# Kernel tuning notes

Hardware: AMD Instinct MI355X
Metric: run time of the kernel (lower is better)

Reference implementation:

```python
import jax, jax.numpy as jnp
import numpy as np
from jax import lax
import math

B, C, H, W, HEADS = 4, 64, 48, 48, 4
CH = C * HEADS
EPS_IN = 1e-5   # InstanceNorm2d eps
EPS_LN = 1e-5   # LayerNorm eps
EPS_NRM = 1e-12 # F.normalize eps


def setup_inputs() -> dict:
    key = jax.random.key(0)
    ks = jax.random.split(key, 8)
    rn = lambda k, shape, s: (jax.random.normal(k, shape, jnp.float32) * s)
    return {
        "emb_all": jax.random.normal(ks[0], (B, C, H, W), jnp.float32),
        "ln_w": jnp.ones((C,), jnp.float32),
        "ln_b": jnp.zeros((C,), jnp.float32),
        "wq": rn(ks[1], (CH, C), 0.05),
        "wk": rn(ks[2], (CH, C), 0.05),
        "wv": rn(ks[3], (CH, C), 0.05),
        "dwq": rn(ks[4], (CH, 1, 3, 3), 0.1),
        "dwk": rn(ks[5], (CH, 1, 3, 3), 0.1),
        "dwv": rn(ks[6], (CH, 1, 3, 3), 0.1),
        "proj_w": rn(ks[7], (C, C), 0.05),
        "proj_b": jnp.zeros((C,), jnp.float32),
    }


def _layernorm_c(x, w, b):
    # Restormer-style 'WithBias' LayerNorm over channel dim of NCHW
    mu = jnp.mean(x, axis=1, keepdims=True)
    var = jnp.mean((x - mu) ** 2, axis=1, keepdims=True)
    xn = (x - mu) / jnp.sqrt(var + EPS_LN)
    return xn * w[None, :, None, None] + b[None, :, None, None]


def _dwconv3(x, k):
    # depthwise 3x3, padding=1, NCHW / OIHW
    return lax.conv_general_dilated(
        x, k, window_strides=(1, 1), padding="SAME",
        feature_group_count=CH,
        dimension_numbers=("NCHW", "OIHW", "NCHW"))


def _qkv_branch(x, w1x1, dw):
    y = jnp.einsum("bchw,oc->bohw", x, w1x1)          # 1x1 conv, no bias
    y = _dwconv3(y, dw)                                # depthwise 3x3
    # b (head c) h w -> b head (h w) c
    y = y.reshape(B, HEADS, C, H * W).transpose(0, 1, 3, 2)
    return y


def reference(emb_all, ln_w, ln_b, wq, wk, wv, dwq, dwk, dwv, proj_w, proj_b):
    org = emb_all
    x = _layernorm_c(emb_all, ln_w, ln_b)

    q = _qkv_branch(x, wq, dwq)   # (B, HEADS, HW, C)
    k = _qkv_branch(x, wk, dwk)
    v = _qkv_branch(x, wv, dwv)

    # L2-normalize along channel dim (F.normalize semantics)
    q = q / jnp.maximum(jnp.linalg.norm(q, axis=-1, keepdims=True), EPS_NRM)
    k = k / jnp.maximum(jnp.linalg.norm(k, axis=-1, keepdims=True), EPS_NRM)

    num = H * W
    atten = jnp.einsum("bhnc,bhmc->bhnm", q, k) / math.sqrt(num)

    # InstanceNorm2d over the (hw x hw) score map, per (batch, head), no affine
    mu = jnp.mean(atten, axis=(-2, -1), keepdims=True)
    var = jnp.mean((atten - mu) ** 2, axis=(-2, -1), keepdims=True)
    atten = (atten - mu) / jnp.sqrt(var + EPS_IN)

    probs = jax.nn.softmax(atten, axis=-1)

    out = jnp.einsum("bhnm,bhmc->bhnc", probs, v)      # (B, HEADS, HW, C)
    out = out.mean(axis=1)                             # average over heads
    out = out.transpose(0, 2, 1).reshape(B, C, H, W)   # b (h w) c -> b c h w
    out = jnp.einsum("bchw,oc->bohw", out, proj_w) + proj_b[None, :, None, None]
    return org + out
```

## Files before the change

kernel.cpp:

```cpp
#include <hip/hip_runtime.h>
#include <hip/hip_bf16.h>
#include <math.h>

#define NB 4
#define NC 64
#define NH 48
#define NW 48
#define NHEADS 4
#define NCH 256
#define NHW 2304
#define NBH 16
#define NCHK 4
#define CHUNK 576
#define NT (CHUNK / 32)

#define OB_Y    0ull
#define OB_G    0ull
#define OB_SQ   524288ull
#define OB_OHP  0ull
#define OB_Q    18874368ull
#define OB_K    23592960ull
#define OB_V    28311552ull
#define OB_L    33030144ull
#define OB_SC   33619968ull

typedef __bf16 bf16x8 __attribute__((ext_vector_type(8)));
typedef float f32x4 __attribute__((ext_vector_type(4)));
typedef float f32x16 __attribute__((ext_vector_type(16)));

__device__ __forceinline__ float bf2f(ushort u) {
  return __uint_as_float(((unsigned)u) << 16);
}
__device__ __forceinline__ ushort f2bf(float f) {
  __hip_bfloat16 h = __float2bfloat16(f);
  return *(ushort*)&h;
}
__device__ __forceinline__ void gload16(const void* g, void* l) {
  __builtin_amdgcn_global_load_lds((const __attribute__((address_space(1))) unsigned int*)g,
                                   (__attribute__((address_space(3))) unsigned int*)l, 16, 0, 0);
}

__global__ __launch_bounds__(256) void k_lnconv(const float* __restrict__ emb,
                                                const float* __restrict__ lw,
                                                const float* __restrict__ lb,
                                                const float* __restrict__ wq,
                                                const float* __restrict__ wk,
                                                const float* __restrict__ wv,
                                                ushort* __restrict__ Y) {
  __shared__ float Xs[64][68];
  __shared__ float mu_s[64], rs_s[64], lw_s[64], lb_s[64];
  int p0 = blockIdx.x * 64, b = blockIdx.y, qkv = blockIdx.z;
  const float* Wm = qkv == 0 ? wq : (qkv == 1 ? wk : wv);
  const float* src = emb + (size_t)b * NC * NHW + p0;
  int t = threadIdx.x;
  for (int e = t; e < 1024; e += 256) {
    int c = e >> 4, p4 = (e & 15) * 4;
    float4 v = *(const float4*)&src[c * NHW + p4];
    Xs[p4][c] = v.x; Xs[p4 + 1][c] = v.y; Xs[p4 + 2][c] = v.z; Xs[p4 + 3][c] = v.w;
  }
  if (t < 64) { lw_s[t] = lw[t]; lb_s[t] = lb[t]; }
  __syncthreads();
  if (t < 64) {
    float s = 0.f, ss = 0.f;
#pragma unroll
    for (int c = 0; c < 64; c += 4) {
      float4 v = *(const float4*)&Xs[t][c];
      s += (v.x + v.y) + (v.z + v.w);
      ss += (v.x * v.x + v.y * v.y) + (v.z * v.z + v.w * v.w);
    }
    float m = s * (1.f / 64.f), va = ss * (1.f / 64.f) - m * m;
    mu_s[t] = m;
    rs_s[t] = rsqrtf(va + 1e-5f);
  }
  __syncthreads();
  int lane = t & 63, wvi = t >> 6, ql = lane & 31, h = lane >> 5;
  bf16x8 bfr[2][4];
#pragma unroll
  for (int pb = 0; pb < 2; ++pb) {
    int px = pb * 32 + ql;
    float mu = mu_s[px], rs = rs_s[px];
#pragma unroll
    for (int kc = 0; kc < 4; ++kc) {
      union { bf16x8 v; ushort u[8]; } pk;
#pragma unroll
      for (int j = 0; j < 8; ++j) {
        int c = kc * 16 + h * 8 + j;
        pk.u[j] = f2bf((Xs[px][c] - mu) * rs * lw_s[c] + lb_s[c]);
      }
      bfr[pb][kc] = pk.v;
    }
  }
  bf16x8 afr[2][4];
#pragma unroll
  for (int ob = 0; ob < 2; ++ob) {
    const float* wr = Wm + (size_t)(wvi * 64 + ob * 32 + ql) * 64;
#pragma unroll
    for (int kc = 0; kc < 4; ++kc) {
      union { bf16x8 v; ushort u[8]; } pk;
#pragma unroll
      for (int j = 0; j < 8; ++j) pk.u[j] = f2bf(wr[kc * 16 + h * 8 + j]);
      afr[ob][kc] = pk.v;
    }
  }
  f32x16 d00 = {}, d01 = {}, d10 = {}, d11 = {};
#pragma unroll
  for (int kc = 0; kc < 4; ++kc) {
    d00 = __builtin_amdgcn_mfma_f32_32x32x16_bf16(afr[0][kc], bfr[0][kc], d00, 0, 0, 0);
    d01 = __builtin_amdgcn_mfma_f32_32x32x16_bf16(afr[0][kc], bfr[1][kc], d01, 0, 0, 0);
    d10 = __builtin_amdgcn_mfma_f32_32x32x16_bf16(afr[1][kc], bfr[0][kc], d10, 0, 0, 0);
    d11 = __builtin_amdgcn_mfma_f32_32x32x16_bf16(afr[1][kc], bfr[1][kc], d11, 0, 0, 0);
  }
  ushort* dst = Y + ((size_t)(qkv * NB + b) * NCH + wvi * 64) * NHW + p0;
#pragma unroll
  for (int r = 0; r < 16; ++r) {
    int row = (r & 3) + 8 * (r >> 2) + 4 * h;
    dst[(size_t)row * NHW + ql] = f2bf(d00[r]);
    dst[(size_t)row * NHW + 32 + ql] = f2bf(d01[r]);
    dst[(size_t)(32 + row) * NHW + ql] = f2bf(d10[r]);
    dst[(size_t)(32 + row) * NHW + 32 + ql] = f2bf(d11[r]);
  }
}

__global__ __launch_bounds__(256) void k_dw(const ushort* __restrict__ Y,
                                            const float* __restrict__ dwq,
                                            const float* __restrict__ dwk,
                                            const float* __restrict__ dwv,
                                            ushort* __restrict__ Qo,
                                            ushort* __restrict__ Ko,
                                            ushort* __restrict__ Vo) {
  __shared__ ushort Ys[64][3][48];
  __shared__ float Zs[64][50];
  __shared__ float Ks9[64][9];
  __shared__ float Rp[4][48];
  __shared__ float Rs[48];
  int h = blockIdx.x;
  int hd = blockIdx.y & 3, qkv = blockIdx.y >> 2;
  int b = blockIdx.z;
  int bh = b * NHEADS + hd;
  const float* dwp = qkv == 0 ? dwq : (qkv == 1 ? dwk : dwv);
  const ushort* src = Y + ((size_t)(qkv * NB + b) * NCH + hd * 64) * NHW;
  int t = threadIdx.x;
  for (int e = t; e < 576; e += 256) Ks9[e / 9][e % 9] = dwp[(size_t)hd * 576 + e];
  for (int e = t; e < 2304; e += 256) {
    int c = e / 36, rem = e % 36, r = rem / 12, w4 = (rem % 12) * 4;
    int hh = h + r - 1;
    ushort4 v = (hh >= 0 && hh < NH) ? *(const ushort4*)&src[c * NHW + hh * NW + w4]
                                     : make_ushort4(0, 0, 0, 0);
    *(ushort4*)&Ys[c][r][w4] = v;
  }
  __syncthreads();
  for (int e = t; e < 768; e += 256) {
    int c = e / 12, w4 = (e % 12) * 4;
    float acc0 = 0.f, acc1 = 0.f, acc2 = 0.f, acc3 = 0.f;
#pragma unroll
    for (int r = 0; r < 3; ++r) {
      const ushort* row = &Ys[c][r][0];
      int li = w4 >= 4 ? w4 - 4 : 0;
      int ri = w4 <= 40 ? w4 + 4 : 40;
      uint2 L = *(const uint2*)&row[li];
      uint2 M = *(const uint2*)&row[w4];
      uint2 R = *(const uint2*)&row[ri];
      float vm1 = (w4 == 0) ? 0.f : __uint_as_float(L.y & 0xffff0000u);
      float m0 = __uint_as_float(M.x << 16);
      float m1 = __uint_as_float(M.x & 0xffff0000u);
      float m2 = __uint_as_float(M.y << 16);
      float m3 = __uint_as_float(M.y & 0xffff0000u);
      float v4 = (w4 == 44) ? 0.f : __uint_as_float(R.x << 16);
      float k0 = Ks9[c][r * 3], k1 = Ks9[c][r * 3 + 1], k2 = Ks9[c][r * 3 + 2];
      acc0 += vm1 * k0 + m0 * k1 + m1 * k2;
      acc1 += m0 * k0 + m1 * k1 + m2 * k2;
      acc2 += m1 * k0 + m2 * k1 + m3 * k2;
      acc3 += m2 * k0 + m3 * k1 + v4 * k2;
    }
    *(float2*)&Zs[c][w4] = make_float2(acc0, acc1);
    *(float2*)&Zs[c][w4 + 2] = make_float2(acc2, acc3);
  }
  __syncthreads();
  if (qkv < 2) {
    if (t < 192) {
      int cq = t / 48, w = t % 48;
      float ss = 0.f;
#pragma unroll
      for (int i = 0; i < 16; ++i) { float z = Zs[cq * 16 + i][w]; ss += z * z; }
      Rp[cq][w] = ss;
    }
    __syncthreads();
    if (t < 48)
      Rs[t] = 1.f / fmaxf(sqrtf(Rp[0][t] + Rp[1][t] + Rp[2][t] + Rp[3][t]), 1e-12f);
    __syncthreads();
    ushort* dst = (qkv == 0 ? Qo : Ko) + (size_t)bh * NHW * 64;
    for (int e = t; e < 768; e += 256) {
      int w = e >> 4, c4 = (e & 15) * 4;
      float rsc = Rs[w];
      ushort4 u = make_ushort4(f2bf(Zs[c4][w] * rsc), f2bf(Zs[c4 + 1][w] * rsc),
                               f2bf(Zs[c4 + 2][w] * rsc), f2bf(Zs[c4 + 3][w] * rsc));
      *(ushort4*)&dst[((size_t)(c4 >> 3) * NHW + h * NW + w) * 8 + (c4 & 7)] = u;
    }
  } else {
    ushort* dst = Vo + (size_t)bh * NHW * 64;
    for (int e = t; e < 768; e += 256) {
      int c = e / 12, w4 = (e % 12) * 4;
      float4 z = *(const float4*)&Zs[c][w4];
      ushort4 u = make_ushort4(f2bf(z.x), f2bf(z.y), f2bf(z.z), f2bf(z.w));
      *(ushort4*)&dst[((size_t)(h * 6 + (w4 >> 3)) * 64 + c) * 8 + (w4 & 7)] = u;
    }
  }
}

__global__ __launch_bounds__(256) void k_gram(const ushort* __restrict__ Q,
                                              const ushort* __restrict__ K,
                                              float* __restrict__ G,
                                              float* __restrict__ SQ) {
  __shared__ ushort Xt[64][72];
  int ns = blockIdx.x, qk = blockIdx.y, bh = blockIdx.z;
  const ushort* src = (qk ? K : Q) + (size_t)bh * NHW * 64;
  int t = threadIdx.x, lane = t & 63, wv = t >> 6;
  int lr = lane & 15, lg = lane >> 4;
  int ci0 = (wv >> 1) * 32, cj0 = (wv & 1) * 32;
  f32x4 acc[2][2];
#pragma unroll
  for (int i = 0; i < 2; ++i)
#pragma unroll
    for (int j = 0; j < 2; ++j) acc[i][j] = (f32x4){0.f, 0.f, 0.f, 0.f};
  float sq = 0.f;
  for (int it = 0; it < 4; ++it) {
    __syncthreads();
#pragma unroll
    for (int i2 = 0; i2 < 2; ++i2) {
      int n = t & 63, cg = (t >> 6) + 4 * i2;
      union { bf16x8 v; ushort u[8]; } ld;
      ld.v = *(const bf16x8*)&src[((size_t)cg * NHW + ns * 256 + it * 64 + n) * 8];
#pragma unroll
      for (int j = 0; j < 8; ++j) Xt[cg * 8 + j][n] = ld.u[j];
    }
    __syncthreads();
    if (t < 64) {
#pragma unroll
      for (int g = 0; g < 8; ++g) {
        union { bf16x8 v; ushort u[8]; } rd;
        rd.v = *(const bf16x8*)&Xt[t][g * 8];
#pragma unroll
        for (int j = 0; j < 8; ++j) sq += bf2f(rd.u[j]);
      }
    }
#pragma unroll
    for (int kh = 0; kh < 2; ++kh) {
      bf16x8 a0 = *(const bf16x8*)&Xt[ci0 + lr][kh * 32 + lg * 8];
      bf16x8 a1 = *(const bf16x8*)&Xt[ci0 + 16 + lr][kh * 32 + lg * 8];
      bf16x8 b0 = *(const bf16x8*)&Xt[cj0 + lr][kh * 32 + lg * 8];
      bf16x8 b1 = *(const bf16x8*)&Xt[cj0 + 16 + lr][kh * 32 + lg * 8];
      acc[0][0] = __builtin_amdgcn_mfma_f32_16x16x32_bf16(a0, b0, acc[0][0], 0, 0, 0);
      acc[0][1] = __builtin_amdgcn_mfma_f32_16x16x32_bf16(a0, b1, acc[0][1], 0, 0, 0);
      acc[1][0] = __builtin_amdgcn_mfma_f32_16x16x32_bf16(a1, b0, acc[1][0], 0, 0, 0);
      acc[1][1] = __builtin_amdgcn_mfma_f32_16x16x32_bf16(a1, b1, acc[1][1], 0, 0, 0);
    }
  }
  float* g = G + ((size_t)qk * NBH + bh) * 4096;
#pragma unroll
  for (int ii = 0; ii < 2; ++ii)
#pragma unroll
    for (int jj = 0; jj < 2; ++jj)
#pragma unroll
      for (int r = 0; r < 4; ++r)
        atomicAdd(&g[(ci0 + ii * 16 + lg * 4 + r) * 64 + cj0 + jj * 16 + lr], acc[ii][jj][r]);
  if (t < 64) atomicAdd(&SQ[((size_t)qk * NBH + bh) * 64 + t], sq);
}

__global__ __launch_bounds__(256) void k_scale(const float* __restrict__ G,
                                               const float* __restrict__ SQ,
                                               float* __restrict__ SC) {
  __shared__ float red[256];
  int bh = blockIdx.x, t = threadIdx.x;
  float ssum = 0.f;
  for (int i = t; i < 4096; i += 256)
    ssum += G[(size_t)bh * 4096 + i] * G[(size_t)(NBH + bh) * 4096 + i];
  red[t] = ssum;
  __syncthreads();
  if (t < 128) red[t] += red[t + 128];
  __syncthreads();
  if (t < 64) {
    float v = red[t] + red[t + 64];
    float v2 = SQ[bh * 64 + t] * SQ[(NBH + bh) * 64 + t];
#pragma unroll
    for (int m = 32; m; m >>= 1) { v += __shfl_xor(v, m); v2 += __shfl_xor(v2, m); }
    if (t == 0) {
      const double N2 = (double)NHW * (double)NHW;
      double mean = (double)v2 / (N2 * 48.0);
      double ea2 = (double)v / (N2 * 2304.0);
      double var = ea2 - mean * mean;
      SC[bh] = (float)((1.0 / sqrt(var + 1e-5)) / 48.0 * 1.4426950408889634);
    }
  }
}

__global__ __launch_bounds__(256, 2) void k_attn(const ushort* __restrict__ Q,
                                                 const ushort* __restrict__ K,
                                                 const ushort* __restrict__ V,
                                                 const float* __restrict__ SC,
                                                 ushort* __restrict__ OHp,
                                                 float* __restrict__ Lp) {
  __shared__ ushort Kl[4][2048];
  __shared__ ushort Vl[4][2048];
  int p = blockIdx.x;
  int gb = p & 7;
  int w = p >> 3;
  int qt = w % 18;
  int rem = w / 18;
  int chunk = rem & 3;
  int bh = gb * 2 + (rem >> 2);
  int t = threadIdx.x, lane = t & 63, wv = t >> 6;
  int ql = lane & 31, h = lane >> 5;
  int q0 = qt * 128 + wv * 32;
  int m00 = chunk * CHUNK;
  const ushort* base = Q + (size_t)bh * NHW * 64;
  float sc2 = SC[bh];

  bf16x8 qfr[4];
#pragma unroll
  for (int kc = 0; kc < 4; ++kc)
    qfr[kc] = *(const bf16x8*)&base[((size_t)(kc * 2 + h) * NHW + q0 + ql) * 8];
  asm volatile("s_waitcnt vmcnt(0)" ::: "memory");

  const ushort* kst = K + (size_t)bh * NHW * 64 + ((size_t)(wv * 2 + h) * NHW + m00 + ql) * 8;
  const ushort* vst = V + (size_t)bh * NHW * 64 + ((size_t)((m00 >> 3) + wv) * 64 + lane) * 8;

  f32x16 o0 = {}, o1 = {};
  float lpA = 0.f, lpB = 0.f;

  auto STAGE = [&](int tt) {
    gload16(kst + (size_t)tt * 256, (void*)&Kl[tt & 3][wv * 512]);
    gload16(vst + (size_t)tt * 2048, (void*)&Vl[tt & 3][wv * 512]);
  };
  auto COMPUTE = [&](int cb, float& lpr) {
    bf16x8 ka[4], vb[4];
#pragma unroll
    for (int i = 0; i < 4; ++i)
      ka[i] = *(const bf16x8*)&Kl[cb][(2 * i + h) * 256 + ql * 8];
    vb[0] = *(const bf16x8*)&Vl[cb][h * 512 + ql * 8];
    vb[1] = *(const bf16x8*)&Vl[cb][(2 + h) * 512 + ql * 8];
    vb[2] = *(const bf16x8*)&Vl[cb][h * 512 + (ql + 32) * 8];
    vb[3] = *(const bf16x8*)&Vl[cb][(2 + h) * 512 + (ql + 32) * 8];
    __builtin_amdgcn_s_setprio(1);
    f32x16 s = {};
    s = __builtin_amdgcn_mfma_f32_32x32x16_bf16(ka[0], qfr[0], s, 0, 0, 0);
    s = __builtin_amdgcn_mfma_f32_32x32x16_bf16(ka[1], qfr[1], s, 0, 0, 0);
    s = __builtin_amdgcn_mfma_f32_32x32x16_bf16(ka[2], qfr[2], s, 0, 0, 0);
    s = __builtin_amdgcn_mfma_f32_32x32x16_bf16(ka[3], qfr[3], s, 0, 0, 0);
    __builtin_amdgcn_s_setprio(0);
    float pv[16];
    float l0 = 0.f, l1 = 0.f, l2 = 0.f, l3 = 0.f;
#pragma unroll
    for (int r = 0; r < 16; r += 4) {
      pv[r] = __builtin_exp2f(s[r] * sc2);
      pv[r + 1] = __builtin_exp2f(s[r + 1] * sc2);
      pv[r + 2] = __builtin_exp2f(s[r + 2] * sc2);
      pv[r + 3] = __builtin_exp2f(s[r + 3] * sc2);
      l0 += pv[r]; l1 += pv[r + 1]; l2 += pv[r + 2]; l3 += pv[r + 3];
    }
    lpr += (l0 + l1) + (l2 + l3);
    uint u[8];
#pragma unroll
    for (int i = 0; i < 8; ++i)
      asm("v_cvt_pk_bf16_f32 %0, %1, %2" : "=v"(u[i]) : "v"(pv[2 * i]), "v"(pv[2 * i + 1]));
    asm volatile("v_permlane32_swap_b32 %0, %1" : "+v"(u[0]), "+v"(u[2]));
    asm volatile("v_permlane32_swap_b32 %0, %1" : "+v"(u[1]), "+v"(u[3]));
    asm volatile("v_permlane32_swap_b32 %0, %1" : "+v"(u[4]), "+v"(u[6]));
    asm volatile("v_permlane32_swap_b32 %0, %1" : "+v"(u[5]), "+v"(u[7]));
    union { uint uu[4]; bf16x8 v; } pa0, pa1;
    pa0.uu[0] = u[0]; pa0.uu[1] = u[1]; pa0.uu[2] = u[2]; pa0.uu[3] = u[3];
    pa1.uu[0] = u[4]; pa1.uu[1] = u[5]; pa1.uu[2] = u[6]; pa1.uu[3] = u[7];
    __builtin_amdgcn_s_setprio(1);
    o0 = __builtin_amdgcn_mfma_f32_32x32x16_bf16(pa0.v, vb[0], o0, 0, 0, 0);
    o0 = __builtin_amdgcn_mfma_f32_32x32x16_bf16(pa1.v, vb[1], o0, 0, 0, 0);
    o1 = __builtin_amdgcn_mfma_f32_32x32x16_bf16(pa0.v, vb[2], o1, 0, 0, 0);
    o1 = __builtin_amdgcn_mfma_f32_32x32x16_bf16(pa1.v, vb[3], o1, 0, 0, 0);
    __builtin_amdgcn_s_setprio(0);
  };

  STAGE(0); STAGE(1);
  for (int mt = 0; mt < NT; mt += 2) {
    asm volatile("s_waitcnt vmcnt(0)" ::: "memory");
    __builtin_amdgcn_s_barrier();
    if (mt + 2 < NT) { STAGE(mt + 2); STAGE(mt + 3); }
    COMPUTE(mt & 3, lpA);
    COMPUTE((mt + 1) & 3, lpB);
  }

  float lp = lpA + lpB;
  lp += __shfl_xor(lp, 32);
  if (h == 0) Lp[(size_t)(chunk * NBH + bh) * NHW + q0 + ql] = lp;
  ushort* od = OHp + ((size_t)(chunk * NBH + bh) * NHW + q0) * 64;
#pragma unroll
  for (int r = 0; r < 16; ++r) {
    int qrow = (r & 3) + 8 * (r >> 2) + 4 * h;
    od[(size_t)qrow * 64 + ql] = f2bf(o0[r]);
    od[(size_t)qrow * 64 + 32 + ql] = f2bf(o1[r]);
  }
}

__global__ __launch_bounds__(256) void k_proj(const ushort* __restrict__ OHp,
                                              const float* __restrict__ Lp,
                                              const float* __restrict__ PW,
                                              const float* __restrict__ PB,
                                              const float* __restrict__ org,
                                              float* __restrict__ out) {
  __shared__ float Ls[4][4][16];
  __shared__ float linv[4][16];
  __shared__ float Ms[64][17];
  int p0 = blockIdx.x * 16, b = blockIdx.y;
  int t = threadIdx.x;
  {
    int ck = t >> 6, hd = (t >> 4) & 3, p = t & 15;
    Ls[ck][hd][p] = Lp[(size_t)(ck * NBH + b * 4 + hd) * NHW + p0 + p];
  }
  __syncthreads();
  if (t < 64) {
    int hd = t >> 4, p = t & 15;
    linv[hd][p] = 1.f / (Ls[0][hd][p] + Ls[1][hd][p] + Ls[2][hd][p] + Ls[3][hd][p]);
  }
  __syncthreads();
  {
    int p = t >> 4, c4 = (t & 15) * 4;
    float a0 = 0.f, a1 = 0.f, a2 = 0.f, a3 = 0.f;
#pragma unroll
    for (int hd = 0; hd < 4; ++hd) {
      float s0 = 0.f, s1 = 0.f, s2 = 0.f, s3 = 0.f;
#pragma unroll
      for (int ck = 0; ck < 4; ++ck) {
        ushort4 u = *(const ushort4*)&OHp[((size_t)(ck * NBH + b * 4 + hd) * NHW + p0 + p) * 64 + c4];
        s0 += bf2f(u.x); s1 += bf2f(u.y); s2 += bf2f(u.z); s3 += bf2f(u.w);
      }
      float li = linv[hd][p];
      a0 += s0 * li; a1 += s1 * li; a2 += s2 * li; a3 += s3 * li;
    }
    Ms[c4][p] = 0.25f * a0;
    Ms[c4 + 1][p] = 0.25f * a1;
    Ms[c4 + 2][p] = 0.25f * a2;
    Ms[c4 + 3][p] = 0.25f * a3;
  }
  __syncthreads();
  int p = t & 15, og = t >> 4;
  float acc[4];
#pragma unroll
  for (int i = 0; i < 4; ++i) acc[i] = PB[og * 4 + i];
  for (int c = 0; c < 64; ++c) {
    float xr = Ms[c][p];
#pragma unroll
    for (int i = 0; i < 4; ++i) acc[i] += PW[(og * 4 + i) * 64 + c] * xr;
  }
  const float* orgp = org + (size_t)b * NC * NHW + p0 + p;
  float* outp = out + (size_t)b * NC * NHW + p0 + p;
#pragma unroll
  for (int i = 0; i < 4; ++i) {
    int oc = og * 4 + i;
    outp[(size_t)oc * NHW] = orgp[(size_t)oc * NHW] + acc[i];
  }
}

extern "C" void kernel_launch(void* const* d_in, const int* in_sizes, int n_in,
                              void* d_out, int out_size, void* d_ws, size_t ws_size,
                              hipStream_t stream) {
  const float* emb = (const float*)d_in[0];
  const float* lnw = (const float*)d_in[1];
  const float* lnb = (const float*)d_in[2];
  const float* wq  = (const float*)d_in[3];
  const float* wk  = (const float*)d_in[4];
  const float* wv  = (const float*)d_in[5];
  const float* dwq = (const float*)d_in[6];
  const float* dwk = (const float*)d_in[7];
  const float* dwv = (const float*)d_in[8];
  const float* pw  = (const float*)d_in[9];
  const float* pb  = (const float*)d_in[10];
  char* ws = (char*)d_ws;
  ushort* Y   = (ushort*)(ws + OB_Y);
  float*  G   = (float*)(ws + OB_G);
  float*  SQ  = (float*)(ws + OB_SQ);
  ushort* OHp = (ushort*)(ws + OB_OHP);
  ushort* Qb  = (ushort*)(ws + OB_Q);
  ushort* Kb  = (ushort*)(ws + OB_K);
  ushort* Vb  = (ushort*)(ws + OB_V);
  float*  Lpt = (float*)(ws + OB_L);
  float*  SCp = (float*)(ws + OB_SC);
  float* out = (float*)d_out;

  k_lnconv<<<dim3(NHW / 64, NB, 3), 256, 0, stream>>>(emb, lnw, lnb, wq, wk, wv, Y);
  k_dw<<<dim3(NH, 12, NB), 256, 0, stream>>>(Y, dwq, dwk, dwv, Qb, Kb, Vb);
  hipMemsetAsync(G, 0, 532480, stream);
  k_gram<<<dim3(9, 2, NBH), 256, 0, stream>>>(Qb, Kb, G, SQ);
  k_scale<<<dim3(NBH), 256, 0, stream>>>(G, SQ, SCp);
  k_attn<<<dim3(1152), 256, 0, stream>>>(Qb, Kb, Vb, SCp, OHp, Lpt);
  k_proj<<<dim3(NHW / 16, NB), 256, 0, stream>>>(OHp, Lpt, pw, pb, emb, out);
}
```

Baseline: 108.7 us.

## Enlarge attention blocks to 8 waves sharing K/V tiles with split loaders

The attention kernel now uses 512-thread blocks covering 256 queries, so each staged K/V tile is reused by eight waves instead of four. Half the waves load K and half load V, one load each per tile. The pipeline moves from double-tile steps with a full vmcnt(0) wait to single-tile steps with a partial vmcnt wait, keeping two tiles in flight. This cuts global K/V traffic and LDS staging per query, at the cost of twice as many barriers and larger-block synchronisation.

```diff
diff --git a/kernel.cpp b/kernel.cpp
--- a/kernel.cpp
+++ b/kernel.cpp
@@ -293,7 +293,7 @@
   }
 }
 
-__global__ __launch_bounds__(256, 2) void k_attn(const ushort* __restrict__ Q,
+__global__ __launch_bounds__(512, 1) void k_attn(const ushort* __restrict__ Q,
                                                  const ushort* __restrict__ K,
                                                  const ushort* __restrict__ V,
                                                  const float* __restrict__ SC,
@@ -304,13 +304,13 @@
   int p = blockIdx.x;
   int gb = p & 7;
   int w = p >> 3;
-  int qt = w % 18;
-  int rem = w / 18;
+  int qt = w % 9;
+  int rem = w / 9;
   int chunk = rem & 3;
   int bh = gb * 2 + (rem >> 2);
   int t = threadIdx.x, lane = t & 63, wv = t >> 6;
   int ql = lane & 31, h = lane >> 5;
-  int q0 = qt * 128 + wv * 32;
+  int q0 = qt * 256 + wv * 32;
   int m00 = chunk * CHUNK;
   const ushort* base = Q + (size_t)bh * NHW * 64;
   float sc2 = SC[bh];
@@ -321,17 +321,21 @@
     qfr[kc] = *(const bf16x8*)&base[((size_t)(kc * 2 + h) * NHW + q0 + ql) * 8];
   asm volatile("s_waitcnt vmcnt(0)" ::: "memory");
 
-  const ushort* kst = K + (size_t)bh * NHW * 64 + ((size_t)(wv * 2 + h) * NHW + m00 + ql) * 8;
-  const ushort* vst = V + (size_t)bh * NHW * 64 + ((size_t)((m00 >> 3) + wv) * 64 + lane) * 8;
+  int sw = wv & 3;
+  bool isK = wv < 4;
+  const ushort* st = isK
+      ? K + (size_t)bh * NHW * 64 + ((size_t)(sw * 2 + h) * NHW + m00 + ql) * 8
+      : V + (size_t)bh * NHW * 64 + ((size_t)((m00 >> 3) + sw) * 64 + lane) * 8;
+  int tstride = isK ? 256 : 2048;
 
   f32x16 o0 = {}, o1 = {};
-  float lpA = 0.f, lpB = 0.f;
+  float lp = 0.f;
 
   auto STAGE = [&](int tt) {
-    gload16(kst + (size_t)tt * 256, (void*)&Kl[tt & 3][wv * 512]);
-    gload16(vst + (size_t)tt * 2048, (void*)&Vl[tt & 3][wv * 512]);
+    void* dst = isK ? (void*)&Kl[tt & 3][sw * 512] : (void*)&Vl[tt & 3][sw * 512];
+    gload16(st + (size_t)tt * tstride, dst);
   };
-  auto COMPUTE = [&](int cb, float& lpr) {
+  auto COMPUTE = [&](int cb) {
     bf16x8 ka[4], vb[4];
 #pragma unroll
     for (int i = 0; i < 4; ++i)
@@ -357,7 +361,7 @@
       pv[r + 3] = __builtin_exp2f(s[r + 3] * sc2);
       l0 += pv[r]; l1 += pv[r + 1]; l2 += pv[r + 2]; l3 += pv[r + 3];
     }
-    lpr += (l0 + l1) + (l2 + l3);
+    lp += (l0 + l1) + (l2 + l3);
     uint u[8];
 #pragma unroll
     for (int i = 0; i < 8; ++i)
@@ -378,15 +382,19 @@
   };
 
   STAGE(0); STAGE(1);
-  for (int mt = 0; mt < NT; mt += 2) {
-    asm volatile("s_waitcnt vmcnt(0)" ::: "memory");
+  for (int mt = 0; mt < NT; ++mt) {
+    if (mt + 2 < NT) {
+      STAGE(mt + 2);
+      asm volatile("s_waitcnt vmcnt(2)" ::: "memory");
+    } else if (mt + 1 < NT) {
+      asm volatile("s_waitcnt vmcnt(1)" ::: "memory");
+    } else {
+      asm volatile("s_waitcnt vmcnt(0)" ::: "memory");
+    }
     __builtin_amdgcn_s_barrier();
-    if (mt + 2 < NT) { STAGE(mt + 2); STAGE(mt + 3); }
-    COMPUTE(mt & 3, lpA);
-    COMPUTE((mt + 1) & 3, lpB);
-  }
-
-  float lp = lpA + lpB;
+    COMPUTE(mt & 3);
+  }
+
   lp += __shfl_xor(lp, 32);
   if (h == 0) Lp[(size_t)(chunk * NBH + bh) * NHW + q0 + ql] = lp;
   ushort* od = OHp + ((size_t)(chunk * NBH + bh) * NHW + q0) * 64;
@@ -488,6 +496,6 @@
   hipMemsetAsync(G, 0, 532480, stream);
   k_gram<<<dim3(9, 2, NBH), 256, 0, stream>>>(Qb, Kb, G, SQ);
   k_scale<<<dim3(NBH), 256, 0, stream>>>(G, SQ, SCp);
-  k_attn<<<dim3(1152), 256, 0, stream>>>(Qb, Kb, Vb, SCp, OHp, Lpt);
+  k_attn<<<dim3(576), 512, 0, stream>>>(Qb, Kb, Vb, SCp, OHp, Lpt);
   k_proj<<<dim3(NHW / 16, NB), 256, 0, stream>>>(OHp, Lpt, pw, pb, emb, out);
 }
```

Result: slower. 111.3 us (+2.4%).

## Fuse layernorm, 1x1 conv, depthwise conv and gram into one kernel; re-pipeline attention loads

Applied to the files above, without the earlier changes.

Merges the layernorm+1x1 conv, depthwise 3x3 conv and Q/K gram-matrix kernels into a single per-row kernel. Each block recomputes the 1x1 conv for its three input rows (a halo of 3 rows per output row), which removes the Y intermediate round trip through global memory and two launches. The gram partials are now accumulated per row with atomics. In exchange the block uses a large LDS pool, which may lower occupancy, and issues more atomic adds. The attention kernel also switches to a single-tile steady-state prefetch loop with a finer vmcnt wait.

```diff
diff --git a/kernel.cpp b/kernel.cpp
--- a/kernel.cpp
+++ b/kernel.cpp
@@ -14,7 +14,6 @@
 #define CHUNK 576
 #define NT (CHUNK / 32)
 
-#define OB_Y    0ull
 #define OB_G    0ull
 #define OB_SQ   524288ull
 #define OB_OHP  0ull
@@ -40,113 +39,126 @@
                                    (__attribute__((address_space(3))) unsigned int*)l, 16, 0, 0);
 }
 
-__global__ __launch_bounds__(256) void k_lnconv(const float* __restrict__ emb,
-                                                const float* __restrict__ lw,
-                                                const float* __restrict__ lb,
-                                                const float* __restrict__ wq,
-                                                const float* __restrict__ wk,
-                                                const float* __restrict__ wv,
-                                                ushort* __restrict__ Y) {
-  __shared__ float Xs[64][68];
-  __shared__ float mu_s[64], rs_s[64], lw_s[64], lb_s[64];
-  int p0 = blockIdx.x * 64, b = blockIdx.y, qkv = blockIdx.z;
-  const float* Wm = qkv == 0 ? wq : (qkv == 1 ? wk : wv);
-  const float* src = emb + (size_t)b * NC * NHW + p0;
-  int t = threadIdx.x;
-  for (int e = t; e < 1024; e += 256) {
-    int c = e >> 4, p4 = (e & 15) * 4;
-    float4 v = *(const float4*)&src[c * NHW + p4];
-    Xs[p4][c] = v.x; Xs[p4 + 1][c] = v.y; Xs[p4 + 2][c] = v.z; Xs[p4 + 3][c] = v.w;
-  }
-  if (t < 64) { lw_s[t] = lw[t]; lb_s[t] = lb[t]; }
-  __syncthreads();
-  if (t < 64) {
-    float s = 0.f, ss = 0.f;
-#pragma unroll
-    for (int c = 0; c < 64; c += 4) {
-      float4 v = *(const float4*)&Xs[t][c];
-      s += (v.x + v.y) + (v.z + v.w);
-      ss += (v.x * v.x + v.y * v.y) + (v.z * v.z + v.w * v.w);
-    }
-    float m = s * (1.f / 64.f), va = ss * (1.f / 64.f) - m * m;
-    mu_s[t] = m;
-    rs_s[t] = rsqrtf(va + 1e-5f);
-  }
-  __syncthreads();
-  int lane = t & 63, wvi = t >> 6, ql = lane & 31, h = lane >> 5;
-  bf16x8 bfr[2][4];
-#pragma unroll
-  for (int pb = 0; pb < 2; ++pb) {
-    int px = pb * 32 + ql;
-    float mu = mu_s[px], rs = rs_s[px];
-#pragma unroll
-    for (int kc = 0; kc < 4; ++kc) {
-      union { bf16x8 v; ushort u[8]; } pk;
-#pragma unroll
-      for (int j = 0; j < 8; ++j) {
-        int c = kc * 16 + h * 8 + j;
-        pk.u[j] = f2bf((Xs[px][c] - mu) * rs * lw_s[c] + lb_s[c]);
-      }
-      bfr[pb][kc] = pk.v;
-    }
-  }
-  bf16x8 afr[2][4];
-#pragma unroll
-  for (int ob = 0; ob < 2; ++ob) {
-    const float* wr = Wm + (size_t)(wvi * 64 + ob * 32 + ql) * 64;
-#pragma unroll
-    for (int kc = 0; kc < 4; ++kc) {
-      union { bf16x8 v; ushort u[8]; } pk;
-#pragma unroll
-      for (int j = 0; j < 8; ++j) pk.u[j] = f2bf(wr[kc * 16 + h * 8 + j]);
-      afr[ob][kc] = pk.v;
-    }
-  }
-  f32x16 d00 = {}, d01 = {}, d10 = {}, d11 = {};
-#pragma unroll
-  for (int kc = 0; kc < 4; ++kc) {
-    d00 = __builtin_amdgcn_mfma_f32_32x32x16_bf16(afr[0][kc], bfr[0][kc], d00, 0, 0, 0);
-    d01 = __builtin_amdgcn_mfma_f32_32x32x16_bf16(afr[0][kc], bfr[1][kc], d01, 0, 0, 0);
-    d10 = __builtin_amdgcn_mfma_f32_32x32x16_bf16(afr[1][kc], bfr[0][kc], d10, 0, 0, 0);
-    d11 = __builtin_amdgcn_mfma_f32_32x32x16_bf16(afr[1][kc], bfr[1][kc], d11, 0, 0, 0);
-  }
-  ushort* dst = Y + ((size_t)(qkv * NB + b) * NCH + wvi * 64) * NHW + p0;
-#pragma unroll
-  for (int r = 0; r < 16; ++r) {
-    int row = (r & 3) + 8 * (r >> 2) + 4 * h;
-    dst[(size_t)row * NHW + ql] = f2bf(d00[r]);
-    dst[(size_t)row * NHW + 32 + ql] = f2bf(d01[r]);
-    dst[(size_t)(32 + row) * NHW + ql] = f2bf(d10[r]);
-    dst[(size_t)(32 + row) * NHW + 32 + ql] = f2bf(d11[r]);
-  }
-}
-
-__global__ __launch_bounds__(256) void k_dw(const ushort* __restrict__ Y,
-                                            const float* __restrict__ dwq,
-                                            const float* __restrict__ dwk,
-                                            const float* __restrict__ dwv,
-                                            ushort* __restrict__ Qo,
-                                            ushort* __restrict__ Ko,
-                                            ushort* __restrict__ Vo) {
-  __shared__ ushort Ys[64][3][48];
-  __shared__ float Zs[64][50];
-  __shared__ float Ks9[64][9];
-  __shared__ float Rp[4][48];
-  __shared__ float Rs[48];
+#define PO_XB 39168
+#define PO_ZS 39168
+#define PO_RP 52768
+#define PO_RS 53536
+#define PO_K9 57600
+#define PO_MU 59904
+#define PO_RSD 60480
+#define PO_LW 61056
+#define PO_LB 61312
+__global__ __launch_bounds__(256) void k_qkv(const float* __restrict__ emb,
+                                             const float* __restrict__ lw,
+                                             const float* __restrict__ lb,
+                                             const float* __restrict__ wq,
+                                             const float* __restrict__ wk,
+                                             const float* __restrict__ wv,
+                                             const float* __restrict__ dwq,
+                                             const float* __restrict__ dwk,
+                                             const float* __restrict__ dwv,
+                                             ushort* __restrict__ Qo,
+                                             ushort* __restrict__ Ko,
+                                             ushort* __restrict__ Vo,
+                                             float* __restrict__ G,
+                                             float* __restrict__ SQ) {
+  __shared__ __align__(16) char pool[61952];
+  float* Xs = (float*)pool;
+  ushort* Yl = (ushort*)pool;
+  float* Zs = (float*)(pool + PO_ZS);
+  float* Rp = (float*)(pool + PO_RP);
+  float* Rs = (float*)(pool + PO_RS);
+  float* Ks9 = (float*)(pool + PO_K9);
+  float* mu_s = (float*)(pool + PO_MU);
+  float* rs_s = (float*)(pool + PO_RSD);
+  float* lw_s = (float*)(pool + PO_LW);
+  float* lb_s = (float*)(pool + PO_LB);
+
   int h = blockIdx.x;
   int hd = blockIdx.y & 3, qkv = blockIdx.y >> 2;
   int b = blockIdx.z;
   int bh = b * NHEADS + hd;
+  const float* Wm = qkv == 0 ? wq : (qkv == 1 ? wk : wv);
   const float* dwp = qkv == 0 ? dwq : (qkv == 1 ? dwk : dwv);
-  const ushort* src = Y + ((size_t)(qkv * NB + b) * NCH + hd * 64) * NHW;
-  int t = threadIdx.x;
-  for (int e = t; e < 576; e += 256) Ks9[e / 9][e % 9] = dwp[(size_t)hd * 576 + e];
+  int t = threadIdx.x, lane = t & 63, wvi = t >> 6;
+  int l15 = lane & 15, l4 = lane >> 4;
+
   for (int e = t; e < 2304; e += 256) {
     int c = e / 36, rem = e % 36, r = rem / 12, w4 = (rem % 12) * 4;
     int hh = h + r - 1;
-    ushort4 v = (hh >= 0 && hh < NH) ? *(const ushort4*)&src[c * NHW + hh * NW + w4]
-                                     : make_ushort4(0, 0, 0, 0);
-    *(ushort4*)&Ys[c][r][w4] = v;
+    float4 v = (hh >= 0 && hh < NH) ? *(const float4*)&emb[((size_t)b * NC + c) * NHW + hh * NW + w4]
+                                    : make_float4(0.f, 0.f, 0.f, 0.f);
+    int p = r * 48 + w4;
+    Xs[p * 68 + c] = v.x;
+    Xs[(p + 1) * 68 + c] = v.y;
+    Xs[(p + 2) * 68 + c] = v.z;
+    Xs[(p + 3) * 68 + c] = v.w;
+  }
+  if (t < 64) { lw_s[t] = lw[t]; lb_s[t] = lb[t]; }
+  for (int e = t; e < 576; e += 256) Ks9[e] = dwp[(size_t)hd * 576 + e];
+  __syncthreads();
+  if (t < 144) {
+    float s = 0.f, ss = 0.f;
+#pragma unroll
+    for (int c = 0; c < 64; c += 4) {
+      float4 v = *(const float4*)&Xs[t * 68 + c];
+      s += (v.x + v.y) + (v.z + v.w);
+      ss += (v.x * v.x + v.y * v.y) + (v.z * v.z + v.w * v.w);
+    }
+    float m = s * (1.f / 64.f), va = ss * (1.f / 64.f) - m * m;
+    mu_s[t] = m;
+    rs_s[t] = rsqrtf(va + 1e-5f);
+  }
+  __syncthreads();
+  for (int e = t; e < 1152; e += 256) {
+    int px = e >> 3, c8 = (e & 7) * 8;
+    int chunk = (c8 >> 3) ^ (px & 7);
+    float mu = mu_s[px], rs = rs_s[px];
+    float4 v0 = *(const float4*)&Xs[px * 68 + c8];
+    float4 v1 = *(const float4*)&Xs[px * 68 + c8 + 4];
+    union { bf16x8 v; ushort u[8]; } pk;
+    pk.u[0] = f2bf((v0.x - mu) * rs * lw_s[c8] + lb_s[c8]);
+    pk.u[1] = f2bf((v0.y - mu) * rs * lw_s[c8 + 1] + lb_s[c8 + 1]);
+    pk.u[2] = f2bf((v0.z - mu) * rs * lw_s[c8 + 2] + lb_s[c8 + 2]);
+    pk.u[3] = f2bf((v0.w - mu) * rs * lw_s[c8 + 3] + lb_s[c8 + 3]);
+    pk.u[4] = f2bf((v1.x - mu) * rs * lw_s[c8 + 4] + lb_s[c8 + 4]);
+    pk.u[5] = f2bf((v1.y - mu) * rs * lw_s[c8 + 5] + lb_s[c8 + 5]);
+    pk.u[6] = f2bf((v1.z - mu) * rs * lw_s[c8 + 6] + lb_s[c8 + 6]);
+    pk.u[7] = f2bf((v1.w - mu) * rs * lw_s[c8 + 7] + lb_s[c8 + 7]);
+    *(bf16x8*)(pool + PO_XB + px * 128 + chunk * 16) = pk.v;
+  }
+  __syncthreads();
+  {
+    bf16x8 afr[2];
+    const float* wr = Wm + (size_t)(hd * 64 + wvi * 16 + l15) * 64;
+#pragma unroll
+    for (int kc = 0; kc < 2; ++kc) {
+      float4 w0 = *(const float4*)&wr[kc * 32 + l4 * 8];
+      float4 w1 = *(const float4*)&wr[kc * 32 + l4 * 8 + 4];
+      union { bf16x8 v; ushort u[8]; } pk;
+      pk.u[0] = f2bf(w0.x); pk.u[1] = f2bf(w0.y); pk.u[2] = f2bf(w0.z); pk.u[3] = f2bf(w0.w);
+      pk.u[4] = f2bf(w1.x); pk.u[5] = f2bf(w1.y); pk.u[6] = f2bf(w1.z); pk.u[7] = f2bf(w1.w);
+      afr[kc] = pk.v;
+    }
+    f32x4 acc[9];
+#pragma unroll
+    for (int i = 0; i < 9; ++i) acc[i] = (f32x4){0.f, 0.f, 0.f, 0.f};
+#pragma unroll
+    for (int pxt = 0; pxt < 9; ++pxt) {
+      int px = pxt * 16 + l15;
+#pragma unroll
+      for (int kc = 0; kc < 2; ++kc) {
+        int chunk = (kc * 4 + l4) ^ (px & 7);
+        bf16x8 bfr = *(const bf16x8*)(pool + PO_XB + px * 128 + chunk * 16);
+        acc[pxt] = __builtin_amdgcn_mfma_f32_16x16x32_bf16(afr[kc], bfr, acc[pxt], 0, 0, 0);
+      }
+    }
+    __syncthreads();
+#pragma unroll
+    for (int pxt = 0; pxt < 9; ++pxt)
+#pragma unroll
+      for (int r = 0; r < 4; ++r)
+        Yl[(wvi * 16 + l4 * 4 + r) * 148 + pxt * 16 + l15] = f2bf(acc[pxt][r]);
   }
   __syncthreads();
   for (int e = t; e < 768; e += 256) {
@@ -154,7 +166,8 @@
     float acc0 = 0.f, acc1 = 0.f, acc2 = 0.f, acc3 = 0.f;
 #pragma unroll
     for (int r = 0; r < 3; ++r) {
-      const ushort* row = &Ys[c][r][0];
+      bool rOK = (unsigned)(h + r - 1) < (unsigned)NH;
+      const ushort* row = &Yl[c * 148 + r * 48];
       int li = w4 >= 4 ? w4 - 4 : 0;
       int ri = w4 <= 40 ? w4 + 4 : 40;
       uint2 L = *(const uint2*)&row[li];
@@ -166,14 +179,16 @@
       float m2 = __uint_as_float(M.y << 16);
       float m3 = __uint_as_float(M.y & 0xffff0000u);
       float v4 = (w4 == 44) ? 0.f : __uint_as_float(R.x << 16);
-      float k0 = Ks9[c][r * 3], k1 = Ks9[c][r * 3 + 1], k2 = Ks9[c][r * 3 + 2];
+      float k0 = rOK ? Ks9[c * 9 + r * 3] : 0.f;
+      float k1 = rOK ? Ks9[c * 9 + r * 3 + 1] : 0.f;
+      float k2 = rOK ? Ks9[c * 9 + r * 3 + 2] : 0.f;
       acc0 += vm1 * k0 + m0 * k1 + m1 * k2;
       acc1 += m0 * k0 + m1 * k1 + m2 * k2;
       acc2 += m1 * k0 + m2 * k1 + m3 * k2;
       acc3 += m2 * k0 + m3 * k1 + v4 * k2;
     }
-    *(float2*)&Zs[c][w4] = make_float2(acc0, acc1);
-    *(float2*)&Zs[c][w4 + 2] = make_float2(acc2, acc3);
+    *(float2*)&Zs[c * 50 + w4] = make_float2(acc0, acc1);
+    *(float2*)&Zs[c * 50 + w4 + 2] = make_float2(acc2, acc3);
   }
   __syncthreads();
   if (qkv < 2) {
@@ -181,89 +196,78 @@
       int cq = t / 48, w = t % 48;
       float ss = 0.f;
 #pragma unroll
-      for (int i = 0; i < 16; ++i) { float z = Zs[cq * 16 + i][w]; ss += z * z; }
-      Rp[cq][w] = ss;
+      for (int i = 0; i < 16; ++i) { float z = Zs[(cq * 16 + i) * 50 + w]; ss += z * z; }
+      Rp[cq * 48 + w] = ss;
     }
     __syncthreads();
     if (t < 48)
-      Rs[t] = 1.f / fmaxf(sqrtf(Rp[0][t] + Rp[1][t] + Rp[2][t] + Rp[3][t]), 1e-12f);
+      Rs[t] = 1.f / fmaxf(sqrtf(Rp[t] + Rp[48 + t] + Rp[96 + t] + Rp[144 + t]), 1e-12f);
     __syncthreads();
     ushort* dst = (qkv == 0 ? Qo : Ko) + (size_t)bh * NHW * 64;
     for (int e = t; e < 768; e += 256) {
       int w = e >> 4, c4 = (e & 15) * 4;
       float rsc = Rs[w];
-      ushort4 u = make_ushort4(f2bf(Zs[c4][w] * rsc), f2bf(Zs[c4 + 1][w] * rsc),
-                               f2bf(Zs[c4 + 2][w] * rsc), f2bf(Zs[c4 + 3][w] * rsc));
+      ushort4 u = make_ushort4(f2bf(Zs[c4 * 50 + w] * rsc), f2bf(Zs[(c4 + 1) * 50 + w] * rsc),
+                               f2bf(Zs[(c4 + 2) * 50 + w] * rsc), f2bf(Zs[(c4 + 3) * 50 + w] * rsc));
       *(ushort4*)&dst[((size_t)(c4 >> 3) * NHW + h * NW + w) * 8 + (c4 & 7)] = u;
+    }
+    for (int e = t; e < 384; e += 256) {
+      int c = e / 6, n8 = (e % 6) * 8;
+      int chunk = (n8 >> 3) ^ (c & 7);
+      union { bf16x8 v; ushort u[8]; } pk;
+#pragma unroll
+      for (int j = 0; j < 8; ++j) pk.u[j] = f2bf(Zs[c * 50 + n8 + j] * Rs[n8 + j]);
+      *(bf16x8*)(pool + c * 128 + chunk * 16) = pk.v;
+    }
+    for (int e = t; e < 128; e += 256) {
+      int c = e >> 1, ch = 6 + (e & 1);
+      int chunk = ch ^ (c & 7);
+      *(bf16x8*)(pool + c * 128 + chunk * 16) = (bf16x8){};
+    }
+    __syncthreads();
+    {
+      int ci0 = wvi * 16;
+      bf16x8 a[2];
+#pragma unroll
+      for (int kc = 0; kc < 2; ++kc) {
+        int row = ci0 + l15;
+        int chunk = (kc * 4 + l4) ^ (row & 7);
+        a[kc] = *(const bf16x8*)(pool + row * 128 + chunk * 16);
+      }
+      f32x4 g[4];
+#pragma unroll
+      for (int i = 0; i < 4; ++i) g[i] = (f32x4){0.f, 0.f, 0.f, 0.f};
+#pragma unroll
+      for (int cj = 0; cj < 4; ++cj) {
+        int row = cj * 16 + l15;
+#pragma unroll
+        for (int kc = 0; kc < 2; ++kc) {
+          int chunk = (kc * 4 + l4) ^ (row & 7);
+          bf16x8 bb = *(const bf16x8*)(pool + row * 128 + chunk * 16);
+          g[cj] = __builtin_amdgcn_mfma_f32_16x16x32_bf16(a[kc], bb, g[cj], 0, 0, 0);
+        }
+      }
+      float* gdst = G + ((size_t)qkv * NBH + bh) * 4096;
+#pragma unroll
+      for (int cj = 0; cj < 4; ++cj)
+#pragma unroll
+        for (int r = 0; r < 4; ++r)
+          atomicAdd(&gdst[(ci0 + l4 * 4 + r) * 64 + cj * 16 + l15], g[cj][r]);
+    }
+    if (t < 64) {
+      float s = 0.f;
+      for (int w = 0; w < 48; ++w) s += bf2f(f2bf(Zs[t * 50 + w] * Rs[w]));
+      atomicAdd(&SQ[((size_t)qkv * NBH + bh) * 64 + t], s);
     }
   } else {
     ushort* dst = Vo + (size_t)bh * NHW * 64;
     for (int e = t; e < 768; e += 256) {
       int c = e / 12, w4 = (e % 12) * 4;
-      float4 z = *(const float4*)&Zs[c][w4];
+      float4 z = *(const float4*)&Zs[c * 50 + w4];
       ushort4 u = make_ushort4(f2bf(z.x), f2bf(z.y), f2bf(z.z), f2bf(z.w));
       *(ushort4*)&dst[((size_t)(h * 6 + (w4 >> 3)) * 64 + c) * 8 + (w4 & 7)] = u;
     }
   }
-}
-
-__global__ __launch_bounds__(256) void k_gram(const ushort* __restrict__ Q,
-                                              const ushort* __restrict__ K,
-                                              float* __restrict__ G,
-                                              float* __restrict__ SQ) {
-  __shared__ ushort Xt[64][72];
-  int ns = blockIdx.x, qk = blockIdx.y, bh = blockIdx.z;
-  const ushort* src = (qk ? K : Q) + (size_t)bh * NHW * 64;
-  int t = threadIdx.x, lane = t & 63, wv = t >> 6;
-  int lr = lane & 15, lg = lane >> 4;
-  int ci0 = (wv >> 1) * 32, cj0 = (wv & 1) * 32;
-  f32x4 acc[2][2];
-#pragma unroll
-  for (int i = 0; i < 2; ++i)
-#pragma unroll
-    for (int j = 0; j < 2; ++j) acc[i][j] = (f32x4){0.f, 0.f, 0.f, 0.f};
-  float sq = 0.f;
-  for (int it = 0; it < 4; ++it) {
-    __syncthreads();
-#pragma unroll
-    for (int i2 = 0; i2 < 2; ++i2) {
-      int n = t & 63, cg = (t >> 6) + 4 * i2;
-      union { bf16x8 v; ushort u[8]; } ld;
-      ld.v = *(const bf16x8*)&src[((size_t)cg * NHW + ns * 256 + it * 64 + n) * 8];
-#pragma unroll
-      for (int j = 0; j < 8; ++j) Xt[cg * 8 + j][n] = ld.u[j];
-    }
-    __syncthreads();
-    if (t < 64) {
-#pragma unroll
-      for (int g = 0; g < 8; ++g) {
-        union { bf16x8 v; ushort u[8]; } rd;
-        rd.v = *(const bf16x8*)&Xt[t][g * 8];
-#pragma unroll
-        for (int j = 0; j < 8; ++j) sq += bf2f(rd.u[j]);
-      }
-    }
-#pragma unroll
-    for (int kh = 0; kh < 2; ++kh) {
-      bf16x8 a0 = *(const bf16x8*)&Xt[ci0 + lr][kh * 32 + lg * 8];
-      bf16x8 a1 = *(const bf16x8*)&Xt[ci0 + 16 + lr][kh * 32 + lg * 8];
-      bf16x8 b0 = *(const bf16x8*)&Xt[cj0 + lr][kh * 32 + lg * 8];
-      bf16x8 b1 = *(const bf16x8*)&Xt[cj0 + 16 + lr][kh * 32 + lg * 8];
-      acc[0][0] = __builtin_amdgcn_mfma_f32_16x16x32_bf16(a0, b0, acc[0][0], 0, 0, 0);
-      acc[0][1] = __builtin_amdgcn_mfma_f32_16x16x32_bf16(a0, b1, acc[0][1], 0, 0, 0);
-      acc[1][0] = __builtin_amdgcn_mfma_f32_16x16x32_bf16(a1, b0, acc[1][0], 0, 0, 0);
-      acc[1][1] = __builtin_amdgcn_mfma_f32_16x16x32_bf16(a1, b1, acc[1][1], 0, 0, 0);
-    }
-  }
-  float* g = G + ((size_t)qk * NBH + bh) * 4096;
-#pragma unroll
-  for (int ii = 0; ii < 2; ++ii)
-#pragma unroll
-    for (int jj = 0; jj < 2; ++jj)
-#pragma unroll
-      for (int r = 0; r < 4; ++r)
-        atomicAdd(&g[(ci0 + ii * 16 + lg * 4 + r) * 64 + cj0 + jj * 16 + lr], acc[ii][jj][r]);
-  if (t < 64) atomicAdd(&SQ[((size_t)qk * NBH + bh) * 64 + t], sq);
 }
 
 __global__ __launch_bounds__(256) void k_scale(const float* __restrict__ G,
@@ -325,13 +329,9 @@
   const ushort* vst = V + (size_t)bh * NHW * 64 + ((size_t)((m00 >> 3) + wv) * 64 + lane) * 8;
 
   f32x16 o0 = {}, o1 = {};
-  float lpA = 0.f, lpB = 0.f;
-
-  auto STAGE = [&](int tt) {
-    gload16(kst + (size_t)tt * 256, (void*)&Kl[tt & 3][wv * 512]);
-    gload16(vst + (size_t)tt * 2048, (void*)&Vl[tt & 3][wv * 512]);
-  };
-  auto COMPUTE = [&](int cb, float& lpr) {
+  float lp = 0.f;
+
+  auto COMPUTE = [&](int cb) {
     bf16x8 ka[4], vb[4];
 #pragma unroll
     for (int i = 0; i < 4; ++i)
@@ -357,7 +357,7 @@
       pv[r + 3] = __builtin_exp2f(s[r + 3] * sc2);
       l0 += pv[r]; l1 += pv[r + 1]; l2 += pv[r + 2]; l3 += pv[r + 3];
     }
-    lpr += (l0 + l1) + (l2 + l3);
+    lp += (l0 + l1) + (l2 + l3);
     uint u[8];
 #pragma unroll
     for (int i = 0; i < 8; ++i)
@@ -377,16 +377,26 @@
     __builtin_amdgcn_s_setprio(0);
   };
 
-  STAGE(0); STAGE(1);
-  for (int mt = 0; mt < NT; mt += 2) {
-    asm volatile("s_waitcnt vmcnt(0)" ::: "memory");
+  gload16(kst, (void*)&Kl[0][wv * 512]);
+  gload16(vst, (void*)&Vl[0][wv * 512]);
+  gload16(kst + 256, (void*)&Kl[1][wv * 512]);
+  gload16(vst + 2048, (void*)&Vl[1][wv * 512]);
+
+  for (int mt = 0; mt < NT - 2; ++mt) {
+    int sb = (mt + 2) & 3;
+    gload16(kst + (size_t)(mt + 2) * 256, (void*)&Kl[sb][wv * 512]);
+    gload16(vst + (size_t)(mt + 2) * 2048, (void*)&Vl[sb][wv * 512]);
+    asm volatile("s_waitcnt vmcnt(4)" ::: "memory");
     __builtin_amdgcn_s_barrier();
-    if (mt + 2 < NT) { STAGE(mt + 2); STAGE(mt + 3); }
-    COMPUTE(mt & 3, lpA);
-    COMPUTE((mt + 1) & 3, lpB);
-  }
-
-  float lp = lpA + lpB;
+    COMPUTE(mt & 3);
+  }
+  asm volatile("s_waitcnt vmcnt(2)" ::: "memory");
+  __builtin_amdgcn_s_barrier();
+  COMPUTE((NT - 2) & 3);
+  asm volatile("s_waitcnt vmcnt(0)" ::: "memory");
+  __builtin_amdgcn_s_barrier();
+  COMPUTE((NT - 1) & 3);
+
   lp += __shfl_xor(lp, 32);
   if (h == 0) Lp[(size_t)(chunk * NBH + bh) * NHW + q0 + ql] = lp;
   ushort* od = OHp + ((size_t)(chunk * NBH + bh) * NHW + q0) * 64;
@@ -472,7 +482,6 @@
   const float* pw  = (const float*)d_in[9];
   const float* pb  = (const float*)d_in[10];
   char* ws = (char*)d_ws;
-  ushort* Y   = (ushort*)(ws + OB_Y);
   float*  G   = (float*)(ws + OB_G);
   float*  SQ  = (float*)(ws + OB_SQ);
   ushort* OHp = (ushort*)(ws + OB_OHP);
@@ -483,10 +492,9 @@
   float*  SCp = (float*)(ws + OB_SC);
   float* out = (float*)d_out;
 
-  k_lnconv<<<dim3(NHW / 64, NB, 3), 256, 0, stream>>>(emb, lnw, lnb, wq, wk, wv, Y);
-  k_dw<<<dim3(NH, 12, NB), 256, 0, stream>>>(Y, dwq, dwk, dwv, Qb, Kb, Vb);
   hipMemsetAsync(G, 0, 532480, stream);
-  k_gram<<<dim3(9, 2, NBH), 256, 0, stream>>>(Qb, Kb, G, SQ);
+  k_qkv<<<dim3(NH, 12, NB), 256, 0, stream>>>(emb, lnw, lnb, wq, wk, wv, dwq, dwk, dwv,
+                                              Qb, Kb, Vb, G, SQ);
   k_scale<<<dim3(NBH), 256, 0, stream>>>(G, SQ, SCp);
   k_attn<<<dim3(1152), 256, 0, stream>>>(Qb, Kb, Vb, SCp, OHp, Lpt);
   k_proj<<<dim3(NHW / 16, NB), 256, 0, stream>>>(OHp, Lpt, pw, pb, emb, out);
```

New measurement: 128.9 us. 18.5% more time.
